# Optimization experiments

Hardware: AMD Instinct MI355X
Metric: run time of the kernel (lower is better)

## Reference

```python
import jax, jax.numpy as jnp
import numpy as np

DIM = 768
NH = 12
HD = DIM // NH  # 64, also the depthwise-pool channel count
SR = 2
EPS_SRN = 1e-6   # sr_norm / up_norm eps
EPS_LN = 1e-5    # default nn.LayerNorm eps for norm_q/k/v


def ln(x, g, b, eps):
    m = x.mean(-1, keepdims=True)
    v = x.var(-1, keepdims=True)
    return (x - m) / jnp.sqrt(v + eps) * g + b


def dwconv(x, w, stride, pad, bias=None):
    # x [N,C,H,W], w [C*m,1,kh,kw] (torch depthwise layout), groups = C
    y = jax.lax.conv_general_dilated(
        x, w, (stride, stride), [(pad, pad), (pad, pad)],
        feature_group_count=x.shape[1],
        dimension_numbers=('NCHW', 'OIHW', 'NCHW'))
    return y if bias is None else y + bias[None, :, None, None]


def setup_inputs() -> dict:
    key = jax.random.key(0)
    ks = jax.random.split(key, 8)
    B, H, W = 8, 56, 56
    N = H * W
    s = 0.02
    f32 = jnp.float32
    d = {
        'x': jax.random.normal(ks[0], (B, N, DIM), f32),
        'q_w': jax.random.normal(ks[1], (DIM, DIM), f32) * s,
        'q_b': jnp.zeros((DIM,), f32),
        'kv_w': jax.random.normal(ks[2], (DIM, 2 * DIM), f32) * s,
        'kv_b': jnp.zeros((2 * DIM,), f32),
        'sr_w': jax.random.normal(ks[3], (DIM, 1, 3, 3), f32) * s,
        'sr_b': jnp.zeros((DIM,), f32),
        'srn_g': jnp.ones((DIM,), f32), 'srn_b': jnp.zeros((DIM,), f32),
        'up_w': jax.random.normal(ks[4], (SR * SR * DIM, 1, 3, 3), f32) * s,
        'up_b': jnp.zeros((SR * SR * DIM,), f32),
        'upn_g': jnp.ones((DIM,), f32), 'upn_b': jnp.zeros((DIM,), f32),
        'proj_w': jax.random.normal(ks[5], (DIM, DIM), f32) * s,
        'proj_b': jnp.zeros((DIM,), f32),
        'pq_w': jax.random.normal(ks[6], (HD, 1, 3, 3), f32) * s,
        'pk_w': jax.random.normal(ks[7], (HD, 1, 3, 3), f32) * s,
        'pv_w': jax.random.normal(jax.random.fold_in(key, 7), (HD, 1, 3, 3), f32) * s,
        'nq_g': jnp.ones((HD,), f32), 'nq_b': jnp.zeros((HD,), f32),
        'nk_g': jnp.ones((HD,), f32), 'nk_b': jnp.zeros((HD,), f32),
        'nv_g': jnp.ones((HD,), f32), 'nv_b': jnp.zeros((HD,), f32),
        'H': H, 'W': W,
    }
    return d


def _forward(x, q_w, q_b, kv_w, kv_b, sr_w, sr_b, srn_g, srn_b,
             up_w, up_b, upn_g, upn_b, proj_w, proj_b,
             pq_w, pk_w, pv_w, nq_g, nq_b, nk_g, nk_b, nv_g, nv_b, H, W):
    B, N, C = x.shape
    scale = HD ** -0.5
    # q projection -> [B, NH, N, HD]
    q = (x @ q_w + q_b).reshape(B, N, NH, HD).transpose(0, 2, 1, 3)
    # pool_q: per-head depthwise 3x3 stride-1 conv + LayerNorm(HD)
    qi = q.reshape(B * NH, H, W, HD).transpose(0, 3, 1, 2)
    qi = dwconv(qi, pq_w, 1, 1)
    q = qi.reshape(B, NH, HD, H * W).transpose(0, 1, 3, 2)
    q = ln(q, nq_g, nq_b, EPS_LN)
    # spatial reduction of x (depthwise k=3, s=2, p=1) + LayerNorm
    xs = x.transpose(0, 2, 1).reshape(B, C, H, W)
    xs = dwconv(xs, sr_w, SR, SR // 2, sr_b)
    Hs, Ws = xs.shape[2], xs.shape[3]  # H//SR, W//SR
    xs = xs.reshape(B, C, Hs * Ws).transpose(0, 2, 1)
    xs = ln(xs, srn_g, srn_b, EPS_SRN)
    # kv projection -> k, v [B, NH, Hs*Ws, HD]
    kv = (xs @ kv_w + kv_b).reshape(B, Hs * Ws, 2, NH, HD).transpose(2, 0, 3, 1, 4)
    k, v = kv[0], kv[1]

    def pool_kv(t, w, g, b):
        ti = t.reshape(B * NH, Hs, Ws, HD).transpose(0, 3, 1, 2)
        ti = dwconv(ti, w, 2, 1)  # stride_kv=(2,2), pad 1
        hk, wk = ti.shape[2], ti.shape[3]
        t2 = ti.reshape(B, NH, HD, hk * wk).transpose(0, 1, 3, 2)
        return ln(t2, g, b, EPS_LN)

    kp = pool_kv(k, pk_w, nk_g, nk_b)
    vp = pool_kv(v, pv_w, nv_g, nv_b)
    # attention core
    attn = jax.nn.softmax(jnp.einsum('bhnd,bhmd->bhnm', q, kp) * scale, axis=-1)
    out = jnp.einsum('bhnm,bhmd->bhnd', attn, vp).transpose(0, 2, 1, 3).reshape(B, N, C)
    # identity path: unpooled v -> depthwise conv -> PixelShuffle(SR) upsample
    idn = v.transpose(0, 1, 3, 2).reshape(B, C, Hs, Ws)
    idn = dwconv(idn, up_w, 1, 1, up_b)  # [B, SR*SR*C, Hs, Ws], groups=C
    idn = idn.reshape(B, C, SR, SR, Hs, Ws).transpose(0, 1, 4, 2, 5, 3).reshape(B, C, Hs * SR, Ws * SR)
    idn = idn.reshape(B, C, N).transpose(0, 2, 1)
    idn = ln(idn, upn_g, upn_b, EPS_SRN)
    return (out + idn) @ proj_w + proj_b


def reference(x, q_w, q_b, kv_w, kv_b, sr_w, sr_b, srn_g, srn_b,
              up_w, up_b, upn_g, upn_b, proj_w, proj_b,
              pq_w, pk_w, pv_w, nq_g, nq_b, nk_g, nk_b, nv_g, nv_b, H, W):
    return _forward(x, q_w, q_b, kv_w, kv_b, sr_w, sr_b, srn_g, srn_b,
                    up_w, up_b, upn_g, upn_b, proj_w, proj_b,
                    pq_w, pk_w, pv_w, nq_g, nq_b, nk_g, nk_b, nv_g, nv_b, H, W)
```

## Files before the change

kernel.cpp:

```cpp
#include <hip/hip_runtime.h>
#include <cstdint>
#include <cstddef>

#define DIM 768
#define NHD 12
#define HD  64
#define HH  56
#define WW  56
#define NQ  3136
#define HS  28
#define WSS 28
#define NS  784
#define HK  14
#define WK  14
#define NKK 196
#define NKP 224
#define VSTR 256

typedef __bf16 bf16x8 __attribute__((ext_vector_type(8)));
typedef __bf16 bf16x4 __attribute__((ext_vector_type(4)));
typedef float  f32x4  __attribute__((ext_vector_type(4)));

__device__ __forceinline__ int xcd_swizzle(int bid, int nwg) {
  const int q = nwg >> 3, r = nwg & 7;
  const int xcd = bid & 7, off = bid >> 3;
  return (xcd < r ? xcd * (q + 1) : r * (q + 1) + (xcd - r) * q) + off;
}

__device__ __forceinline__ void gload_lds16(const void* g, void* l) {
  __builtin_amdgcn_global_load_lds(
      (const __attribute__((address_space(1))) void*)g,
      (__attribute__((address_space(3))) void*)l, 16, 0, 0);
}

#define LDP 48

template<int MODE>
__global__ __launch_bounds__(256) void gemm_mfma_kernel(
    const __bf16* __restrict__ A, const __bf16* __restrict__ Bt,
    const float* __restrict__ bias, float* __restrict__ C,
    __bf16* __restrict__ Cq, int M, int N, int K)
{
  __shared__ __bf16 As[128 * LDP];
  __shared__ __bf16 Bs[128 * LDP];

  const int nX = N >> 7;
  const int bid = xcd_swizzle(blockIdx.x, (M >> 7) * nX);
  const int row0 = (bid / nX) << 7;
  const int col0 = (bid % nX) << 7;

  const int t = threadIdx.x;
  const int lane = t & 63;
  const int w = t >> 6;
  const int wr = w >> 1, wc = w & 1;

  const int rs = t >> 1;
  const int kh = (t & 1) << 4;
  const __bf16* Aptr = A + (size_t)(row0 + rs) * K + kh;
  const __bf16* Bptr = Bt + (size_t)(col0 + rs) * K + kh;

  f32x4 acc[4][4];
#pragma unroll
  for (int i = 0; i < 4; ++i)
#pragma unroll
    for (int j = 0; j < 4; ++j) acc[i][j] = (f32x4){0.f, 0.f, 0.f, 0.f};

  const int fr = lane & 15;
  const int fc = lane >> 4;

  int4 a0 = *(const int4*)(Aptr);
  int4 a1 = *(const int4*)(Aptr + 8);
  int4 b0 = *(const int4*)(Bptr);
  int4 b1 = *(const int4*)(Bptr + 8);

  const int NT = K >> 5;
  for (int kt = 0; kt < NT; ++kt) {
    __syncthreads();
    *(int4*)(&As[rs * LDP + kh]) = a0;
    *(int4*)(&As[rs * LDP + kh + 8]) = a1;
    *(int4*)(&Bs[rs * LDP + kh]) = b0;
    *(int4*)(&Bs[rs * LDP + kh + 8]) = b1;
    __syncthreads();
    if (kt + 1 < NT) {
      const __bf16* ap = Aptr + ((kt + 1) << 5);
      const __bf16* bp = Bptr + ((kt + 1) << 5);
      a0 = *(const int4*)(ap);
      a1 = *(const int4*)(ap + 8);
      b0 = *(const int4*)(bp);
      b1 = *(const int4*)(bp + 8);
    }
    bf16x8 af[4], bfr[4];
#pragma unroll
    for (int i = 0; i < 4; ++i)
      af[i] = *(const bf16x8*)(&As[(wr * 64 + i * 16 + fr) * LDP + fc * 8]);
#pragma unroll
    for (int j = 0; j < 4; ++j)
      bfr[j] = *(const bf16x8*)(&Bs[(wc * 64 + j * 16 + fr) * LDP + fc * 8]);
#pragma unroll
    for (int i = 0; i < 4; ++i)
#pragma unroll
      for (int j = 0; j < 4; ++j)
        acc[i][j] = __builtin_amdgcn_mfma_f32_16x16x32_bf16(af[i], bfr[j], acc[i][j], 0, 0, 0);
  }

  const int orow = row0 + wr * 64 + ((lane >> 4) << 2);
  const int ocol = col0 + wc * 64 + (lane & 15);
#pragma unroll
  for (int j = 0; j < 4; ++j) {
    const int col = ocol + j * 16;
    const float bv = bias[col];
#pragma unroll
    for (int i = 0; i < 4; ++i)
#pragma unroll
      for (int r = 0; r < 4; ++r) {
        const int rrow = orow + i * 16 + r;
        if (MODE == 0) {
          C[(size_t)rrow * N + col] = acc[i][j][r] + bv;
        } else if (MODE == 1) {
          const int b = rrow / NQ, n = rrow - b * NQ;
          const int h = col >> 6, hd = col & 63;
          Cq[(((size_t)b * NHD + h) * NQ + n) * HD + hd] = (__bf16)(acc[i][j][r] + bv);
        } else {
          Cq[(size_t)rrow * N + col] = (__bf16)(acc[i][j][r] + bv);
        }
      }
  }
}

__global__ __launch_bounds__(256) void cast_bf16_kernel(
    const float* __restrict__ in, __bf16* __restrict__ out, long n4)
{
  long i = (long)blockIdx.x * 256 + threadIdx.x;
  const long stride = (long)gridDim.x * 256;
  for (; i < n4; i += stride) {
    float4 v = *(const float4*)(in + i * 4);
    bf16x4 o;
    o.x = (__bf16)v.x; o.y = (__bf16)v.y; o.z = (__bf16)v.z; o.w = (__bf16)v.w;
    *(bf16x4*)(out + i * 4) = o;
  }
}

__global__ __launch_bounds__(256) void wt_cast_kernel(
    const float* __restrict__ W, __bf16* __restrict__ Wt, int K, int N)
{
  __shared__ float tile[32][33];
  const int k0 = blockIdx.y << 5;
  const int n0 = blockIdx.x << 5;
  const int tc = threadIdx.x & 31;
  const int tr = threadIdx.x >> 5;
#pragma unroll
  for (int i = 0; i < 4; ++i)
    tile[tr + i * 8][tc] = W[(size_t)(k0 + tr + i * 8) * N + n0 + tc];
  __syncthreads();
#pragma unroll
  for (int i = 0; i < 4; ++i)
    Wt[(size_t)(n0 + tr + i * 8) * K + k0 + tc] = (__bf16)tile[tc][tr + i * 8];
}

__global__ __launch_bounds__(256) void up_tr_kernel(
    const float* __restrict__ upw, float* __restrict__ upt)
{
  const int i = blockIdx.x * 256 + threadIdx.x;
  if (i < 4 * 9 * DIM) {
    const int c = i % DIM;
    const int rest = i / DIM;
    const int tap = rest % 9, sidx = rest / 9;
    upt[i] = upw[(c * 4 + sidx) * 9 + tap];
  }
}

__global__ __launch_bounds__(256) void sr_tr_kernel(
    const float* __restrict__ srw, float* __restrict__ srt)
{
  const int i = blockIdx.x * 256 + threadIdx.x;
  if (i < 9 * DIM) {
    const int c = i % DIM;
    const int tap = i / DIM;
    srt[i] = srw[c * 9 + tap];
  }
}

__global__ __launch_bounds__(256) void pool_q_ln_kernel(
    const __bf16* __restrict__ qp, const float* __restrict__ pqw,
    const float* __restrict__ g, const float* __restrict__ bb,
    __bf16* __restrict__ qf)
{
  const int blk = xcd_swizzle(blockIdx.x, gridDim.x);
  const int bh = blk / HH, y = blk - bh * HH;
  const int lane = threadIdx.x & 63;
  const int w = threadIdx.x >> 6;
  const int x0 = w * (WW / 4);

  float wt[9];
#pragma unroll
  for (int tap = 0; tap < 9; ++tap) {
    const int yy = y - 1 + tap / 3;
    wt[tap] = (yy >= 0 && yy < HH) ? pqw[lane * 9 + tap] : 0.f;
  }
  const float gl = g[lane], bl = bb[lane];

  const __bf16* rp0;
  const __bf16* rp1;
  const __bf16* rp2;
  {
    const __bf16* base = qp + (size_t)bh * NQ * HD + lane;
    rp0 = base + (size_t)min(max(y - 1, 0), HH - 1) * WW * HD;
    rp1 = base + (size_t)y * WW * HD;
    rp2 = base + (size_t)min(max(y + 1, 0), HH - 1) * WW * HD;
  }
  auto ldc = [&](int xx, float* d) {
    const float m = (xx >= 0 && xx < WW) ? 1.f : 0.f;
    const int xc = min(max(xx, 0), WW - 1);
    d[0] = m * (float)rp0[(size_t)xc * HD];
    d[1] = m * (float)rp1[(size_t)xc * HD];
    d[2] = m * (float)rp2[(size_t)xc * HD];
  };

  float c0[3], c1[3], c2[3], cn[3];
  ldc(x0 - 1, c0);
  ldc(x0,     c1);
  ldc(x0 + 1, c2);

#pragma unroll
  for (int xi = 0; xi < WW / 4; ++xi) {
    const int x = x0 + xi;
    ldc(x + 2, cn);
    float acc = 0.f;
#pragma unroll
    for (int dy = 0; dy < 3; ++dy) {
      acc = fmaf(wt[dy * 3 + 0], c0[dy], acc);
      acc = fmaf(wt[dy * 3 + 1], c1[dy], acc);
      acc = fmaf(wt[dy * 3 + 2], c2[dy], acc);
    }
    float s = acc, sq = acc * acc;
#pragma unroll
    for (int off = 32; off > 0; off >>= 1) {
      s  += __shfl_xor(s, off);
      sq += __shfl_xor(sq, off);
    }
    const float mean = s * (1.f / 64.f);
    const float var  = sq * (1.f / 64.f) - mean * mean;
    const float rstd = rsqrtf(var + 1e-5f);
    qf[((size_t)bh * NQ + y * WW + x) * HD + lane] =
        (__bf16)((acc - mean) * rstd * gl + bl);
#pragma unroll
    for (int dy = 0; dy < 3; ++dy) {
      c0[dy] = c1[dy]; c1[dy] = c2[dy]; c2[dy] = cn[dy];
    }
  }
}

__global__ __launch_bounds__(256) void sr_ln_kernel(
    const __bf16* __restrict__ x, const float* __restrict__ srt,
    const float* __restrict__ srb, const float* __restrict__ g,
    const float* __restrict__ bb, __bf16* __restrict__ out)
{
  const int row = xcd_swizzle(blockIdx.x, gridDim.x);
  const int b = row / NS, ns = row - b * NS;
  const int ys = ns / WSS, xs = ns - ys * WSS;
  const int t = threadIdx.x;

  float fm[9];
  size_t off9[9];
#pragma unroll
  for (int tap = 0; tap < 9; ++tap) {
    const int yy = 2 * ys - 1 + tap / 3;
    const int xx = 2 * xs - 1 + tap % 3;
    fm[tap] = (yy >= 0 && yy < HH && xx >= 0 && xx < WW) ? 1.f : 0.f;
    const int yyc = min(max(yy, 0), HH - 1);
    const int xxc = min(max(xx, 0), WW - 1);
    off9[tap] = ((size_t)b * NQ + yyc * WW + xxc) * DIM;
  }

  float vals[3];
  float lsum = 0.f, lsq = 0.f;
#pragma unroll
  for (int i = 0; i < 3; ++i) {
    const int c = t + i * 256;
    float v9[9];
#pragma unroll
    for (int tap = 0; tap < 9; ++tap) v9[tap] = (float)x[off9[tap] + c];
    float acc = srb[c];
#pragma unroll
    for (int tap = 0; tap < 9; ++tap)
      acc = fmaf(srt[tap * DIM + c] * fm[tap], v9[tap], acc);
    vals[i] = acc;
    lsum += acc;
    lsq = fmaf(acc, acc, lsq);
  }
#pragma unroll
  for (int off = 32; off > 0; off >>= 1) {
    lsum += __shfl_xor(lsum, off);
    lsq  += __shfl_xor(lsq, off);
  }
  __shared__ float s1[4], s2[4];
  if ((t & 63) == 0) { s1[t >> 6] = lsum; s2[t >> 6] = lsq; }
  __syncthreads();
  const float S  = s1[0] + s1[1] + s1[2] + s1[3];
  const float SQ = s2[0] + s2[1] + s2[2] + s2[3];
  const float mean = S * (1.f / 768.f);
  const float var  = SQ * (1.f / 768.f) - mean * mean;
  const float rstd = rsqrtf(var + 1e-6f);
#pragma unroll
  for (int i = 0; i < 3; ++i) {
    const int c = t + i * 256;
    out[(size_t)row * DIM + c] = (__bf16)((vals[i] - mean) * rstd * g[c] + bb[c]);
  }
}

__global__ __launch_bounds__(256) void pool_kv_ln_kernel(
    const __bf16* __restrict__ kv, const float* __restrict__ pkw,
    const float* __restrict__ pvw, const float* __restrict__ kg,
    const float* __restrict__ kbb, const float* __restrict__ vg,
    const float* __restrict__ vbb, __bf16* __restrict__ kpb,
    __bf16* __restrict__ vtb)
{
  const int isv = blockIdx.y;
  const float* pw = isv ? pvw : pkw;
  const float* g  = isv ? vg  : kg;
  const float* bb = isv ? vbb : kbb;
  const int coloff = isv ? DIM : 0;

  const int lane = threadIdx.x & 63;
  const int r = blockIdx.x * 4 + (threadIdx.x >> 6);
  const int bh = r / NKP;
  const int nk = r - bh * NKP;

  float val = 0.f;
  if (nk < NKK) {
    const int b = bh / NHD, h = bh - b * NHD;
    const int yk = nk / WK, xk = nk - yk * WK;
    float acc = 0.f;
#pragma unroll
    for (int dy = 0; dy < 3; ++dy) {
      const int yy = 2 * yk - 1 + dy;
      if (yy < 0 || yy >= HS) continue;
#pragma unroll
      for (int dx = 0; dx < 3; ++dx) {
        const int xx = 2 * xk - 1 + dx;
        if (xx < 0 || xx >= WSS) continue;
        acc = fmaf(pw[lane * 9 + dy * 3 + dx],
                   (float)kv[((size_t)b * NS + yy * WSS + xx) * (2 * DIM) + coloff + h * HD + lane], acc);
      }
    }
    float s = acc, sq = acc * acc;
#pragma unroll
    for (int off = 32; off > 0; off >>= 1) {
      s  += __shfl_xor(s, off);
      sq += __shfl_xor(sq, off);
    }
    const float mean = s * (1.f / 64.f);
    const float var  = sq * (1.f / 64.f) - mean * mean;
    const float rstd = rsqrtf(var + 1e-5f);
    val = (acc - mean) * rstd * g[lane] + bb[lane];
  }
  if (!isv) {
    kpb[(size_t)bh * NKP * HD + nk * HD + (lane ^ ((nk & 7) << 3))] = (__bf16)val;
  } else {
    vtb[(size_t)bh * HD * VSTR + lane * VSTR + (nk ^ ((lane & 7) << 3))] = (__bf16)val;
  }
}

__global__ __launch_bounds__(256) void attn_mfma_kernel(
    const __bf16* __restrict__ qf, const __bf16* __restrict__ kpb,
    const __bf16* __restrict__ vtb, __bf16* __restrict__ out)
{
  __shared__ __bf16 kp_lds[16384];
  __shared__ __bf16 v_lds[16384];
  const int bh = blockIdx.y;
  const int qt = blockIdx.x;
  const int t = threadIdx.x;
  const int lane = t & 63, w = t >> 6;
  const int fr = lane & 15;
  const int fg = lane >> 4;
  const int q0 = qt * 64 + w * 16;
  const int sw = (fr & 7) << 4;

  const __bf16* qbase = qf + ((size_t)bh * NQ + q0) * HD;
  const bf16x8 aq0 = *(const bf16x8*)(qbase + fr * HD + fg * 8);
  const bf16x8 aq1 = *(const bf16x8*)(qbase + fr * HD + 32 + fg * 8);

  {
    const __bf16* kgp = kpb + (size_t)bh * (NKP * HD);
    const __bf16* vgp = vtb + (size_t)bh * (HD * VSTR);
    char* kl = (char*)kp_lds;
    char* vl = (char*)v_lds;
#pragma unroll
    for (int i = 0; i < 7; ++i)
      gload_lds16(kgp + (i * 256 + w * 64 + lane) * 8, kl + i * 4096 + w * 1024);
#pragma unroll
    for (int i = 0; i < 8; ++i)
      gload_lds16(vgp + (i * 256 + w * 64 + lane) * 8, vl + i * 4096 + w * 1024);
  }
  __syncthreads();

  const char* kl = (const char*)kp_lds;
  f32x4 s[13];
#pragma unroll
  for (int n = 0; n < 13; ++n) {
    const int rowb = (n * 16 + fr) << 7;
    const bf16x8 b0 = *(const bf16x8*)(kl + rowb + ((fg << 4) ^ sw));
    const bf16x8 b1 = *(const bf16x8*)(kl + rowb + (((fg << 4) + 64) ^ sw));
    f32x4 c = (f32x4){0.f, 0.f, 0.f, 0.f};
    c = __builtin_amdgcn_mfma_f32_16x16x32_bf16(aq0, b0, c, 0, 0, 0);
    c = __builtin_amdgcn_mfma_f32_16x16x32_bf16(aq1, b1, c, 0, 0, 0);
    s[n] = c;
  }
  __syncthreads();

  const float scale = 0.125f;
  char* pb = (char*)kp_lds;
  float pinv[4];
#pragma unroll
  for (int r = 0; r < 4; ++r) {
    const int row = 4 * fg + r;
    const int rbase = (w * 16 + row) * (VSTR * 2);
    const int rsw = (row & 7) << 4;
    float sum = 0.f;
#pragma unroll
    for (int n = 0; n < 13; ++n) {
      float e = __expf(s[n][r] * scale);
      if (n == 12 && fr >= 4) e = 0.f;
      *(__bf16*)(pb + rbase + ((((n * 16 + fr) << 1)) ^ rsw)) = (__bf16)e;
      sum += e;
    }
    *(__bf16*)(pb + rbase + ((((208 + fr) << 1)) ^ rsw)) = (__bf16)0.f;
    sum += __shfl_xor(sum, 1);
    sum += __shfl_xor(sum, 2);
    sum += __shfl_xor(sum, 4);
    sum += __shfl_xor(sum, 8);
    pinv[r] = 1.f / sum;
  }

  f32x4 acc2[4];
#pragma unroll
  for (int dt = 0; dt < 4; ++dt) acc2[dt] = (f32x4){0.f, 0.f, 0.f, 0.f};
  const char* vl = (const char*)v_lds;
#pragma unroll
  for (int ks = 0; ks < 7; ++ks) {
    const bf16x8 pabf = *(const bf16x8*)(pb + (w * 16 + fr) * (VSTR * 2) + ((ks * 64 + (fg << 4)) ^ sw));
#pragma unroll
    for (int dt = 0; dt < 4; ++dt) {
      const bf16x8 bv = *(const bf16x8*)(vl + (dt * 16 + fr) * (VSTR * 2) + ((ks * 64 + (fg << 4)) ^ sw));
      acc2[dt] = __builtin_amdgcn_mfma_f32_16x16x32_bf16(pabf, bv, acc2[dt], 0, 0, 0);
    }
  }

  const int b = bh / NHD, h = bh - b * NHD;
#pragma unroll
  for (int dt = 0; dt < 4; ++dt)
#pragma unroll
    for (int r = 0; r < 4; ++r)
      out[((size_t)b * NQ + q0 + 4 * fg + r) * DIM + h * HD + dt * 16 + fr] =
          (__bf16)(acc2[dt][r] * pinv[r]);
}

#define XCH 2

__global__ __launch_bounds__(256) void idn_add_ln_kernel(
    const __bf16* __restrict__ kv, const float* __restrict__ upt,
    const float* __restrict__ upb, const float* __restrict__ g,
    const float* __restrict__ bb, const __bf16* __restrict__ io,
    __bf16* __restrict__ pj)
{
  int idx = xcd_swizzle(blockIdx.x, gridDim.x);
  const int chunk = idx & (XCH - 1); idx >>= 1;
  const int ys = idx % HS; idx /= HS;
  const int sidx = idx & 3;
  const int b = idx >> 2;
  const int sy = sidx >> 1, sx = sidx & 1;
  const int y = 2 * ys + sy;
  const int t = threadIdx.x;
  const int w = t >> 6;

  float wreg[3][9], ubias[3], gg[3], gb[3];
#pragma unroll
  for (int i = 0; i < 3; ++i) {
    const int c = t + i * 256;
    ubias[i] = upb[c * 4 + sidx];
    gg[i] = g[c];
    gb[i] = bb[c];
#pragma unroll
    for (int tap = 0; tap < 9; ++tap) {
      const int yy = ys - 1 + tap / 3;
      const float f = (yy >= 0 && yy < HS) ? 1.f : 0.f;
      wreg[i][tap] = upt[(sidx * 9 + tap) * DIM + c] * f;
    }
  }

  __shared__ __bf16 vals_lds[14][DIM];
  __shared__ float s1[14][4], s2[14][4];
  const int xs0 = chunk * 14;

  const int y0 = max(ys - 1, 0), y1 = ys, y2 = min(ys + 1, HS - 1);
  const __bf16* vb0 = kv + ((size_t)(b * NS + y0 * WSS)) * (2 * DIM) + DIM + t;
  const __bf16* vb1 = kv + ((size_t)(b * NS + y1 * WSS)) * (2 * DIM) + DIM + t;
  const __bf16* vb2 = kv + ((size_t)(b * NS + y2 * WSS)) * (2 * DIM) + DIM + t;

  auto ldcol = [&](int ch, int p, float* dst) {
    const float m = (p >= 0 && p < WSS) ? 1.f : 0.f;
    const int xx = min(max(p, 0), WSS - 1);
    const size_t off = (size_t)xx * (2 * DIM) + ch * 256;
    dst[0] = m * (float)vb0[off];
    dst[1] = m * (float)vb1[off];
    dst[2] = m * (float)vb2[off];
  };

  float c0[3][3], c1[3][3], c2[3][3], cn[3][3];
#pragma unroll
  for (int ch = 0; ch < 3; ++ch) {
    ldcol(ch, xs0 - 1, c0[ch]);
    ldcol(ch, xs0,     c1[ch]);
    ldcol(ch, xs0 + 1, c2[ch]);
  }

#pragma unroll
  for (int xi = 0; xi < 14; ++xi) {
    const int xs = xs0 + xi;
#pragma unroll
    for (int ch = 0; ch < 3; ++ch) ldcol(ch, xs + 2, cn[ch]);
    float lsum = 0.f, lsq = 0.f;
#pragma unroll
    for (int ch = 0; ch < 3; ++ch) {
      float acc = ubias[ch];
#pragma unroll
      for (int dy = 0; dy < 3; ++dy) {
        acc = fmaf(wreg[ch][dy * 3 + 0], c0[ch][dy], acc);
        acc = fmaf(wreg[ch][dy * 3 + 1], c1[ch][dy], acc);
        acc = fmaf(wreg[ch][dy * 3 + 2], c2[ch][dy], acc);
      }
      vals_lds[xi][t + ch * 256] = (__bf16)acc;
      lsum += acc;
      lsq = fmaf(acc, acc, lsq);
    }
#pragma unroll
    for (int off = 32; off > 0; off >>= 1) {
      lsum += __shfl_xor(lsum, off);
      lsq  += __shfl_xor(lsq, off);
    }
    if ((t & 63) == 0) { s1[xi][w] = lsum; s2[xi][w] = lsq; }
#pragma unroll
    for (int ch = 0; ch < 3; ++ch)
#pragma unroll
      for (int dy = 0; dy < 3; ++dy) {
        c0[ch][dy] = c1[ch][dy];
        c1[ch][dy] = c2[ch][dy];
        c2[ch][dy] = cn[ch][dy];
      }
  }
  __syncthreads();

#pragma unroll
  for (int xi = 0; xi < 14; ++xi) {
    const float S  = s1[xi][0] + s1[xi][1] + s1[xi][2] + s1[xi][3];
    const float SQ = s2[xi][0] + s2[xi][1] + s2[xi][2] + s2[xi][3];
    const float mean = S * (1.f / 768.f);
    const float var  = SQ * (1.f / 768.f) - mean * mean;
    const float rstd = rsqrtf(var + 1e-6f);
    const int x = 2 * (xs0 + xi) + sx;
    const size_t row = (size_t)b * NQ + y * WW + x;
#pragma unroll
    for (int ch = 0; ch < 3; ++ch) {
      const int c = t + ch * 256;
      pj[row * DIM + c] =
          (__bf16)((float)io[row * DIM + c] +
                   ((float)vals_lds[xi][c] - mean) * rstd * gg[ch] + gb[ch]);
    }
  }
}

extern "C" void kernel_launch(void* const* d_in, const int* in_sizes, int n_in,
                              void* d_out, int out_size, void* d_ws, size_t ws_size,
                              hipStream_t stream)
{
  const float* x      = (const float*)d_in[0];
  const float* q_w    = (const float*)d_in[1];
  const float* q_b    = (const float*)d_in[2];
  const float* kv_w   = (const float*)d_in[3];
  const float* kv_b   = (const float*)d_in[4];
  const float* sr_w   = (const float*)d_in[5];
  const float* sr_b   = (const float*)d_in[6];
  const float* srn_g  = (const float*)d_in[7];
  const float* srn_b  = (const float*)d_in[8];
  const float* up_w   = (const float*)d_in[9];
  const float* up_b   = (const float*)d_in[10];
  const float* upn_g  = (const float*)d_in[11];
  const float* upn_b  = (const float*)d_in[12];
  const float* proj_w = (const float*)d_in[13];
  const float* proj_b = (const float*)d_in[14];
  const float* pq_w   = (const float*)d_in[15];
  const float* pk_w   = (const float*)d_in[16];
  const float* pv_w   = (const float*)d_in[17];
  const float* nq_g   = (const float*)d_in[18];
  const float* nq_b   = (const float*)d_in[19];
  const float* nk_g   = (const float*)d_in[20];
  const float* nk_b   = (const float*)d_in[21];
  const float* nv_g   = (const float*)d_in[22];
  const float* nv_b   = (const float*)d_in[23];

  const int B = in_sizes[0] / (NQ * DIM);
  const int M1 = B * NQ;
  const int M2 = B * NS;

  char* p = (char*)d_ws;
  __bf16* xb    = (__bf16*)p;  p += (size_t)M1 * DIM * 2;
  float*  qproj = (float*)p;   p += (size_t)M1 * DIM * 4;
  __bf16* qf    = (__bf16*)p;  p += (size_t)M1 * DIM * 2;
  __bf16* xsln  = (__bf16*)p;  p += (size_t)M2 * DIM * 2;
  __bf16* kvb   = (__bf16*)p;  p += (size_t)M2 * 2 * DIM * 2;
  __bf16* kpb   = (__bf16*)p;  p += (size_t)B * NHD * NKP * HD * 2;
  __bf16* vtb   = (__bf16*)p;  p += (size_t)B * NHD * HD * VSTR * 2;
  __bf16* wqt   = (__bf16*)p;  p += (size_t)DIM * DIM * 2;
  __bf16* wkvt  = (__bf16*)p;  p += (size_t)DIM * 2 * DIM * 2;
  __bf16* wpjt  = (__bf16*)p;  p += (size_t)DIM * DIM * 2;
  float*  upt   = (float*)p;   p += (size_t)4 * 9 * DIM * 4;
  float*  srt   = (float*)p;   p += (size_t)9 * DIM * 4;
  __bf16* qp      = (__bf16*)qproj;
  __bf16* attnout = (__bf16*)qproj;
  __bf16* pjin    = xb;

  dim3 blk(256);

  cast_bf16_kernel<<<2048, blk, 0, stream>>>(x, xb, (long)M1 * DIM / 4);
  wt_cast_kernel<<<dim3(DIM / 32, DIM / 32), blk, 0, stream>>>(q_w, wqt, DIM, DIM);
  wt_cast_kernel<<<dim3(2 * DIM / 32, DIM / 32), blk, 0, stream>>>(kv_w, wkvt, DIM, 2 * DIM);
  wt_cast_kernel<<<dim3(DIM / 32, DIM / 32), blk, 0, stream>>>(proj_w, wpjt, DIM, DIM);
  up_tr_kernel<<<(4 * 9 * DIM + 255) / 256, blk, 0, stream>>>(up_w, upt);
  sr_tr_kernel<<<(9 * DIM + 255) / 256, blk, 0, stream>>>(sr_w, srt);

  gemm_mfma_kernel<1><<<(M1 / 128) * (DIM / 128), blk, 0, stream>>>(
      xb, wqt, q_b, nullptr, qp, M1, DIM, DIM);

  pool_q_ln_kernel<<<B * NHD * HH, blk, 0, stream>>>(
      qp, pq_w, nq_g, nq_b, qf);

  sr_ln_kernel<<<B * NS, blk, 0, stream>>>(
      xb, srt, sr_b, srn_g, srn_b, xsln);

  gemm_mfma_kernel<2><<<(M2 / 128) * (2 * DIM / 128), blk, 0, stream>>>(
      xsln, wkvt, kv_b, nullptr, kvb, M2, 2 * DIM, DIM);

  pool_kv_ln_kernel<<<dim3((B * NHD * NKP) / 4, 2), blk, 0, stream>>>(
      kvb, pk_w, pv_w, nk_g, nk_b, nv_g, nv_b, kpb, vtb);

  attn_mfma_kernel<<<dim3(NQ / 64, B * NHD), blk, 0, stream>>>(
      qf, kpb, vtb, attnout);

  idn_add_ln_kernel<<<B * 4 * HS * XCH, blk, 0, stream>>>(
      kvb, upt, up_b, upn_g, upn_b, attnout, pjin);

  gemm_mfma_kernel<0><<<(M1 / 128) * (DIM / 128), blk, 0, stream>>>(
      pjin, wpjt, proj_b, (float*)d_out, nullptr, M1, DIM, DIM);
}
```

Measured before the change: 331.5 us.

## Use direct-to-LDS loads with swizzle in GEMM and read V from global in attention

The GEMM kernel drops register-staged tile loads with a padded LDS layout. It now uses global_load_lds 16-byte transfers into an unpadded, XOR-swizzled 32-wide LDS tile, which removes the register prefetch and shrinks LDS. In the attention kernel, the V tile is no longer staged through LDS: V is stored unswizzled with a 224 stride and MFMA operands are read straight from global memory. This halves attention LDS use, which may raise occupancy. The cost is that the GEMM loses its overlap of next-tile loads with compute, and attention adds uncoalesced global reads of V inside the inner loop.

```diff
diff --git a/kernel.cpp b/kernel.cpp
--- a/kernel.cpp
+++ b/kernel.cpp
@@ -15,7 +15,8 @@
 #define WK  14
 #define NKK 196
 #define NKP 224
-#define VSTR 256
+#define VSTR 224
+#define PROWB 512
 
 typedef __bf16 bf16x8 __attribute__((ext_vector_type(8)));
 typedef __bf16 bf16x4 __attribute__((ext_vector_type(4)));
@@ -32,8 +33,6 @@
       (const __attribute__((address_space(1))) void*)g,
       (__attribute__((address_space(3))) void*)l, 16, 0, 0);
 }
-
-#define LDP 48
 
 template<int MODE>
 __global__ __launch_bounds__(256) void gemm_mfma_kernel(
@@ -41,8 +40,8 @@
     const float* __restrict__ bias, float* __restrict__ C,
     __bf16* __restrict__ Cq, int M, int N, int K)
 {
-  __shared__ __bf16 As[128 * LDP];
-  __shared__ __bf16 Bs[128 * LDP];
+  __shared__ __bf16 As[128 * 32];
+  __shared__ __bf16 Bs[128 * 32];
 
   const int nX = N >> 7;
   const int bid = xcd_swizzle(blockIdx.x, (M >> 7) * nX);
@@ -53,49 +52,49 @@
   const int lane = t & 63;
   const int w = t >> 6;
   const int wr = w >> 1, wc = w & 1;
-
-  const int rs = t >> 1;
-  const int kh = (t & 1) << 4;
-  const __bf16* Aptr = A + (size_t)(row0 + rs) * K + kh;
-  const __bf16* Bptr = Bt + (size_t)(col0 + rs) * K + kh;
-
-  f32x4 acc[4][4];
-#pragma unroll
-  for (int i = 0; i < 4; ++i)
-#pragma unroll
-    for (int j = 0; j < 4; ++j) acc[i][j] = (f32x4){0.f, 0.f, 0.f, 0.f};
-
   const int fr = lane & 15;
   const int fc = lane >> 4;
 
-  int4 a0 = *(const int4*)(Aptr);
-  int4 a1 = *(const int4*)(Aptr + 8);
-  int4 b0 = *(const int4*)(Bptr);
-  int4 b1 = *(const int4*)(Bptr + 8);
+  const int r0 = t >> 2;
+  const int ch = t & 3;
+  const int sc = ch ^ ((r0 >> 1) & 3);
+  const __bf16* Ap0 = A + (size_t)(row0 + r0) * K + sc * 8;
+  const __bf16* Ap1 = A + (size_t)(row0 + r0 + 64) * K + sc * 8;
+  const __bf16* Bp0 = Bt + (size_t)(col0 + r0) * K + sc * 8;
+  const __bf16* Bp1 = Bt + (size_t)(col0 + r0 + 64) * K + sc * 8;
+  char* Asb = (char*)As;
+  char* Bsb = (char*)Bs;
+  const int db = w * 1024;
+
+  f32x4 acc[4][4];
+#pragma unroll
+  for (int i = 0; i < 4; ++i)
+#pragma unroll
+    for (int j = 0; j < 4; ++j) acc[i][j] = (f32x4){0.f, 0.f, 0.f, 0.f};
+
+  const int keyA = (fr >> 1) & 3;
 
   const int NT = K >> 5;
   for (int kt = 0; kt < NT; ++kt) {
+    const int ko = kt << 5;
     __syncthreads();
-    *(int4*)(&As[rs * LDP + kh]) = a0;
-    *(int4*)(&As[rs * LDP + kh + 8]) = a1;
-    *(int4*)(&Bs[rs * LDP + kh]) = b0;
-    *(int4*)(&Bs[rs * LDP + kh + 8]) = b1;
+    gload_lds16(Ap0 + ko, Asb + db);
+    gload_lds16(Ap1 + ko, Asb + 4096 + db);
+    gload_lds16(Bp0 + ko, Bsb + db);
+    gload_lds16(Bp1 + ko, Bsb + 4096 + db);
     __syncthreads();
-    if (kt + 1 < NT) {
-      const __bf16* ap = Aptr + ((kt + 1) << 5);
-      const __bf16* bp = Bptr + ((kt + 1) << 5);
-      a0 = *(const int4*)(ap);
-      a1 = *(const int4*)(ap + 8);
-      b0 = *(const int4*)(bp);
-      b1 = *(const int4*)(bp + 8);
-    }
+
     bf16x8 af[4], bfr[4];
 #pragma unroll
-    for (int i = 0; i < 4; ++i)
-      af[i] = *(const bf16x8*)(&As[(wr * 64 + i * 16 + fr) * LDP + fc * 8]);
-#pragma unroll
-    for (int j = 0; j < 4; ++j)
-      bfr[j] = *(const bf16x8*)(&Bs[(wc * 64 + j * 16 + fr) * LDP + fc * 8]);
+    for (int i = 0; i < 4; ++i) {
+      const int r = wr * 64 + i * 16 + fr;
+      af[i] = *(const bf16x8*)(Asb + r * 64 + ((fc ^ keyA) << 4));
+    }
+#pragma unroll
+    for (int j = 0; j < 4; ++j) {
+      const int r = wc * 64 + j * 16 + fr;
+      bfr[j] = *(const bf16x8*)(Bsb + r * 64 + ((fc ^ keyA) << 4));
+    }
 #pragma unroll
     for (int i = 0; i < 4; ++i)
 #pragma unroll
@@ -357,7 +356,7 @@
   if (!isv) {
     kpb[(size_t)bh * NKP * HD + nk * HD + (lane ^ ((nk & 7) << 3))] = (__bf16)val;
   } else {
-    vtb[(size_t)bh * HD * VSTR + lane * VSTR + (nk ^ ((lane & 7) << 3))] = (__bf16)val;
+    vtb[(size_t)bh * HD * VSTR + lane * VSTR + nk] = (__bf16)val;
   }
 }
 
@@ -366,7 +365,6 @@
     const __bf16* __restrict__ vtb, __bf16* __restrict__ out)
 {
   __shared__ __bf16 kp_lds[16384];
-  __shared__ __bf16 v_lds[16384];
   const int bh = blockIdx.y;
   const int qt = blockIdx.x;
   const int t = threadIdx.x;
@@ -382,15 +380,10 @@
 
   {
     const __bf16* kgp = kpb + (size_t)bh * (NKP * HD);
-    const __bf16* vgp = vtb + (size_t)bh * (HD * VSTR);
     char* kl = (char*)kp_lds;
-    char* vl = (char*)v_lds;
 #pragma unroll
     for (int i = 0; i < 7; ++i)
       gload_lds16(kgp + (i * 256 + w * 64 + lane) * 8, kl + i * 4096 + w * 1024);
-#pragma unroll
-    for (int i = 0; i < 8; ++i)
-      gload_lds16(vgp + (i * 256 + w * 64 + lane) * 8, vl + i * 4096 + w * 1024);
   }
   __syncthreads();
 
@@ -414,7 +407,7 @@
 #pragma unroll
   for (int r = 0; r < 4; ++r) {
     const int row = 4 * fg + r;
-    const int rbase = (w * 16 + row) * (VSTR * 2);
+    const int rbase = (w * 16 + row) * PROWB;
     const int rsw = (row & 7) << 4;
     float sum = 0.f;
 #pragma unroll
@@ -435,13 +428,13 @@
   f32x4 acc2[4];
 #pragma unroll
   for (int dt = 0; dt < 4; ++dt) acc2[dt] = (f32x4){0.f, 0.f, 0.f, 0.f};
-  const char* vl = (const char*)v_lds;
+  const __bf16* vb = vtb + (size_t)bh * HD * VSTR;
 #pragma unroll
   for (int ks = 0; ks < 7; ++ks) {
-    const bf16x8 pabf = *(const bf16x8*)(pb + (w * 16 + fr) * (VSTR * 2) + ((ks * 64 + (fg << 4)) ^ sw));
+    const bf16x8 pabf = *(const bf16x8*)(pb + (w * 16 + fr) * PROWB + ((ks * 64 + (fg << 4)) ^ sw));
 #pragma unroll
     for (int dt = 0; dt < 4; ++dt) {
-      const bf16x8 bv = *(const bf16x8*)(vl + (dt * 16 + fr) * (VSTR * 2) + ((ks * 64 + (fg << 4)) ^ sw));
+      const bf16x8 bv = *(const bf16x8*)(vb + (size_t)(dt * 16 + fr) * VSTR + ks * 32 + fg * 8);
       acc2[dt] = __builtin_amdgcn_mfma_f32_16x16x32_bf16(pabf, bv, acc2[dt], 0, 0, 0);
     }
   }
```

New measurement: 356.3 us. +7.5%, slower.
